# Kernel tuning notes

Measured on AMD Instinct MI355X. Metric: run time of the kernel, lower is better.

## Reference

```python
import jax, jax.numpy as jnp
import numpy as np

N_NODES = 100000
DEG = 32  # in-degree per node


def setup_inputs() -> dict:
    key = jax.random.key(0)
    ks = jax.random.split(key, 8)
    E = N_NODES * DEG
    x = jax.random.normal(ks[0], (N_NODES, 4), dtype=jnp.float32)
    src = jax.random.randint(ks[1], (E,), 0, N_NODES, dtype=jnp.int32)
    # every node gets exactly DEG incoming messages (DGL mean-reduce semantics)
    dst = jnp.repeat(jnp.arange(N_NODES, dtype=jnp.int32), DEG)
    s = 0.3
    return {
        "x": x, "src": src, "dst": dst,
        "W1": jax.random.normal(ks[2], (4, 32), jnp.float32) * s,
        "b1": jax.random.normal(ks[3], (32,), jnp.float32) * s,
        "W2": jax.random.normal(ks[4], (32, 32), jnp.float32) * s,
        "b2": jax.random.normal(ks[5], (32,), jnp.float32) * s,
        "W3": jax.random.normal(ks[6], (32, 1), jnp.float32) * s,
        "b3": jax.random.normal(ks[7], (1,), jnp.float32) * s,
    }


def _gcn_layer(h, src, dst, deg_inv, W, b):
    # copy_src: gather source features per edge, mean-reduce by destination
    m = jax.ops.segment_sum(h[src], dst, num_segments=N_NODES)
    h_mean = m * deg_inv  # [N, F_in]
    # node apply: ReLU(W h + b)
    return jax.nn.relu(h_mean @ W + b)


def reference(x, src, dst, W1, b1, W2, b2, W3, b3):
    ones = jnp.ones((src.shape[0],), x.dtype)
    deg = jax.ops.segment_sum(ones, dst, num_segments=N_NODES)
    deg_inv = (1.0 / jnp.maximum(deg, 1.0))[:, None]
    h = _gcn_layer(x, src, dst, deg_inv, W1, b1)   # [N, 32]
    h = _gcn_layer(h, src, dst, deg_inv, W2, b2)   # [N, 32]
    h = _gcn_layer(h, src, dst, deg_inv, W3, b3)   # [N, 1]
    return h
```

## Files before the change

### kernel.cpp

```cpp
#include <hip/hip_runtime.h>
#include <hip/hip_bf16.h>

#define N_NODES 100000
#define DEG 32

__global__ __launch_bounds__(256) void gcn_l1(const float* __restrict__ x,
                                              const int* __restrict__ src,
                                              const float* __restrict__ W1,
                                              const float* __restrict__ b1,
                                              __hip_bfloat16* __restrict__ h1) {
    int tid  = blockIdx.x * 256 + threadIdx.x;
    int node = tid >> 5;
    if (node >= N_NODES) return;
    int lane = threadIdx.x & 31;

    int s = src[node * DEG + lane];
    const float4 v = *reinterpret_cast<const float4*>(x + (size_t)s * 4);
    float m0 = v.x, m1 = v.y, m2 = v.z, m3 = v.w;
#pragma unroll
    for (int off = 16; off; off >>= 1) {
        m0 += __shfl_xor(m0, off, 32);
        m1 += __shfl_xor(m1, off, 32);
        m2 += __shfl_xor(m2, off, 32);
        m3 += __shfl_xor(m3, off, 32);
    }
    const float inv = 1.0f / 32.0f;
    m0 *= inv; m1 *= inv; m2 *= inv; m3 *= inv;

    float o = b1[lane];
    o = fmaf(m0, W1[0 * 32 + lane], o);
    o = fmaf(m1, W1[1 * 32 + lane], o);
    o = fmaf(m2, W1[2 * 32 + lane], o);
    o = fmaf(m3, W1[3 * 32 + lane], o);
    h1[(size_t)node * 32 + lane] = __float2bfloat16(fmaxf(o, 0.0f));
}

__global__ __launch_bounds__(256) void gcn_l2(const __hip_bfloat16* __restrict__ h1,
                                              const int* __restrict__ src,
                                              const float* __restrict__ W2,
                                              const float* __restrict__ b2,
                                              const float* __restrict__ W3,
                                              float* __restrict__ g) {
    __shared__ float sW2[32 * 32];
    for (int i = threadIdx.x; i < 1024; i += 256) sW2[i] = W2[i];
    __syncthreads();

    int tid  = blockIdx.x * 256 + threadIdx.x;
    int node = tid >> 5;
    if (node >= N_NODES) return;
    int lane = threadIdx.x & 31;

    int sv = src[node * DEG + lane];

    float acc = 0.0f;
#pragma unroll
    for (int k = 0; k < 32; ++k) {
        int s = __shfl(sv, k, 32);
        acc += __bfloat162float(h1[(size_t)s * 32 + lane]);
    }
    float m = acc * (1.0f / 32.0f);

    float o = b2[lane];
#pragma unroll
    for (int k = 0; k < 32; ++k) {
        o = fmaf(__shfl(m, k, 32), sW2[k * 32 + lane], o);
    }
    float h2 = fmaxf(o, 0.0f);

    float p = h2 * W3[lane];
#pragma unroll
    for (int off = 16; off; off >>= 1) p += __shfl_xor(p, off, 32);
    if (lane == 0) g[node] = p;
}

__global__ __launch_bounds__(256) void gcn_l3(const float* __restrict__ g,
                                              const int* __restrict__ src,
                                              const float* __restrict__ b3,
                                              float* __restrict__ out) {
    int tid  = blockIdx.x * 256 + threadIdx.x;
    int node = tid >> 5;
    if (node >= N_NODES) return;
    int lane = threadIdx.x & 31;

    float p = g[src[node * DEG + lane]];
#pragma unroll
    for (int off = 16; off; off >>= 1) p += __shfl_xor(p, off, 32);
    if (lane == 0) out[node] = fmaxf(p * (1.0f / 32.0f) + b3[0], 0.0f);
}

extern "C" void kernel_launch(void* const* d_in, const int* in_sizes, int n_in,
                              void* d_out, int out_size, void* d_ws, size_t ws_size,
                              hipStream_t stream) {
    const float* x   = (const float*)d_in[0];
    const int*   src = (const int*)d_in[1];
    const float* W1  = (const float*)d_in[3];
    const float* b1  = (const float*)d_in[4];
    const float* W2  = (const float*)d_in[5];
    const float* b2  = (const float*)d_in[6];
    const float* W3  = (const float*)d_in[7];
    const float* b3  = (const float*)d_in[8];
    float* out = (float*)d_out;

    __hip_bfloat16* h1 = (__hip_bfloat16*)d_ws;
    float* g = (float*)((char*)d_ws + (size_t)N_NODES * 32 * sizeof(__hip_bfloat16));

    dim3 block(256);
    dim3 grid((N_NODES * DEG + 255) / 256);
    gcn_l1<<<grid, block, 0, stream>>>(x, src, W1, b1, h1);
    gcn_l2<<<grid, block, 0, stream>>>(h1, src, W2, b2, W3, g);
    gcn_l3<<<grid, block, 0, stream>>>(g, src, b3, out);
}
```

Baseline: 161.1 us.

## Restructure layer-2 kernel: 64 nodes per block, 16-byte bf16 gathers, shared-memory matvec

Layer 2 now processes 64 nodes per block. Source indices are staged in shared memory with vectorized int4 loads, and each node's 64-byte bf16 row is gathered as four 16-byte loads (4 threads per node) instead of 32 two-byte loads. Mean features are transposed into padded shared memory. Each wavefront then computes 8 output channels of the 32x32 matvec per node, with W3 projection partials reduced through shared memory. This cuts memory transactions and shuffle work in the dominant gather kernel, at the cost of more shared memory and extra block-level synchronisation.

```diff
diff --git a/kernel.cpp b/kernel.cpp
--- a/kernel.cpp
+++ b/kernel.cpp
@@ -3,6 +3,14 @@
 
 #define N_NODES 100000
 #define DEG 32
+#define E_TOTAL (3200000LL)
+
+static __device__ __forceinline__ float bf16_lo(unsigned int u) {
+    return __uint_as_float(u << 16);
+}
+static __device__ __forceinline__ float bf16_hi(unsigned int u) {
+    return __uint_as_float(u & 0xffff0000u);
+}
 
 __global__ __launch_bounds__(256) void gcn_l1(const float* __restrict__ x,
                                               const int* __restrict__ src,
@@ -41,36 +49,85 @@
                                               const float* __restrict__ b2,
                                               const float* __restrict__ W3,
                                               float* __restrict__ g) {
-    __shared__ float sW2[32 * 32];
-    for (int i = threadIdx.x; i < 1024; i += 256) sW2[i] = W2[i];
+    __shared__ int   sidx[64 * 36];
+    __shared__ float mt[64 * 33];
+    __shared__ float gpart[4 * 65];
+
+    const int t  = threadIdx.x;
+    const long long n0 = (long long)blockIdx.x * 64;
+
+    {
+        long long j = n0 * DEG + (long long)t * 8;
+        int4 v0, v1;
+        if (j + 7 < E_TOTAL) {
+            v0 = *reinterpret_cast<const int4*>(src + j);
+            v1 = *reinterpret_cast<const int4*>(src + j + 4);
+        } else {
+            int tmp[8];
+#pragma unroll
+            for (int m = 0; m < 8; ++m) tmp[m] = (j + m < E_TOTAL) ? src[j + m] : 0;
+            v0 = make_int4(tmp[0], tmp[1], tmp[2], tmp[3]);
+            v1 = make_int4(tmp[4], tmp[5], tmp[6], tmp[7]);
+        }
+        int jn = t >> 2;
+        int k0 = (t & 3) * 8;
+        *reinterpret_cast<int4*>(&sidx[jn * 36 + k0])     = v0;
+        *reinterpret_cast<int4*>(&sidx[jn * 36 + k0 + 4]) = v1;
+    }
     __syncthreads();
 
-    int tid  = blockIdx.x * 256 + threadIdx.x;
-    int node = tid >> 5;
-    if (node >= N_NODES) return;
-    int lane = threadIdx.x & 31;
+    {
+        const int nl = t >> 2;
+        const int q  = t & 3;
+        const int sb = nl * 36;
+        float a0 = 0.f, a1 = 0.f, a2 = 0.f, a3 = 0.f, a4 = 0.f, a5 = 0.f, a6 = 0.f, a7 = 0.f;
+        const char* hbase = (const char*)h1 + q * 16;
+#pragma unroll
+        for (int k = 0; k < 32; ++k) {
+            int s = sidx[sb + k];
+            const uint4 u = *reinterpret_cast<const uint4*>(hbase + ((size_t)(unsigned)s << 6));
+            a0 += bf16_lo(u.x); a1 += bf16_hi(u.x);
+            a2 += bf16_lo(u.y); a3 += bf16_hi(u.y);
+            a4 += bf16_lo(u.z); a5 += bf16_hi(u.z);
+            a6 += bf16_lo(u.w); a7 += bf16_hi(u.w);
+        }
+        const float inv = 1.0f / 32.0f;
+        const int mb = nl * 33 + q * 8;
+        mt[mb + 0] = a0 * inv; mt[mb + 1] = a1 * inv;
+        mt[mb + 2] = a2 * inv; mt[mb + 3] = a3 * inv;
+        mt[mb + 4] = a4 * inv; mt[mb + 5] = a5 * inv;
+        mt[mb + 6] = a6 * inv; mt[mb + 7] = a7 * inv;
+    }
+    __syncthreads();
 
-    int sv = src[node * DEG + lane];
+    {
+        const int w = __builtin_amdgcn_readfirstlane(t >> 6);
+        const int l = t & 63;
+        const float* __restrict__ b2w = b2 + w * 8;
+        const float* __restrict__ w3w = W3 + w * 8;
+        float o[8];
+#pragma unroll
+        for (int j = 0; j < 8; ++j) o[j] = b2w[j];
+        const int rb = l * 33;
+#pragma unroll
+        for (int k = 0; k < 32; ++k) {
+            const float mk = mt[rb + k];
+            const float* __restrict__ w2r = W2 + k * 32 + w * 8;
+#pragma unroll
+            for (int j = 0; j < 8; ++j) o[j] = fmaf(mk, w2r[j], o[j]);
+        }
+        float p = 0.f;
+#pragma unroll
+        for (int j = 0; j < 8; ++j) p += fmaxf(o[j], 0.f) * w3w[j];
+        gpart[w * 65 + l] = p;
+    }
+    __syncthreads();
 
-    float acc = 0.0f;
-#pragma unroll
-    for (int k = 0; k < 32; ++k) {
-        int s = __shfl(sv, k, 32);
-        acc += __bfloat162float(h1[(size_t)s * 32 + lane]);
+    if (t < 64) {
+        float s = gpart[t] + gpart[65 + t] + gpart[130 + t] + gpart[195 + t];
+        long long node = n0 + t;
+        if (node < N_NODES) g[node] = s;
     }
-    float m = acc * (1.0f / 32.0f);
-
-    float o = b2[lane];
-#pragma unroll
-    for (int k = 0; k < 32; ++k) {
-        o = fmaf(__shfl(m, k, 32), sW2[k * 32 + lane], o);
-    }
-    float h2 = fmaxf(o, 0.0f);
-
-    float p = h2 * W3[lane];
-#pragma unroll
-    for (int off = 16; off; off >>= 1) p += __shfl_xor(p, off, 32);
-    if (lane == 0) g[node] = p;
 }
 
 __global__ __launch_bounds__(256) void gcn_l3(const float* __restrict__ g,
@@ -105,8 +162,7 @@
     float* g = (float*)((char*)d_ws + (size_t)N_NODES * 32 * sizeof(__hip_bfloat16));
 
     dim3 block(256);
-    dim3 grid((N_NODES * DEG + 255) / 256);
-    gcn_l1<<<grid, block, 0, stream>>>(x, src, W1, b1, h1);
-    gcn_l2<<<grid, block, 0, stream>>>(h1, src, W2, b2, W3, g);
-    gcn_l3<<<grid, block, 0, stream>>>(g, src, b3, out);
+    gcn_l1<<<dim3((N_NODES * DEG + 255) / 256), block, 0, stream>>>(x, src, W1, b1, h1);
+    gcn_l2<<<dim3((N_NODES + 63) / 64),        block, 0, stream>>>(h1, src, W2, b2, W3, g);
+    gcn_l3<<<dim3((N_NODES * DEG + 255) / 256), block, 0, stream>>>(g, src, b3, out);
 }
```

After: 142.6 us. 1.13x faster.
